# Performance work log

Measured on AMD Instinct MI355X. Metric: run time of the kernel, lower is better.

Reference implementation:

```python
import jax, jax.numpy as jnp
import numpy as np
from jax import lax

B, S, T = 64, 50, 50
U, E = 1024, 256
VI, VT = 12000, 16000
BOS = 1


def _gru_step(h, x, Wx, Wh, b):
    # Keras GRU v2 (reset_after=True): b[0]=input bias, b[1]=recurrent bias
    gi = x @ Wx + b[0]          # [B, 3U]
    gh = h @ Wh + b[1]          # [B, 3U]
    iz, ir, ih = jnp.split(gi, 3, axis=-1)
    hz, hr, hh = jnp.split(gh, 3, axis=-1)
    z = jax.nn.sigmoid(iz + hz)
    r = jax.nn.sigmoid(ir + hr)
    hcand = jnp.tanh(ih + r * hh)
    return z * h + (1.0 - z) * hcand


def setup_inputs() -> dict:
    key = jax.random.key(0)
    ks = jax.random.split(key, 20)
    f = lambda k, shp: (jax.random.normal(k, shp, dtype=jnp.float32) * 0.05)
    inp = jax.random.randint(ks[0], (B, S), 0, VI)
    targ = jax.random.randint(ks[1], (B, T), 0, VT)
    targ = targ.at[:, 0].set(BOS)  # <bos> first token (teacher forcing input)
    return {
        'inp': inp,
        'targ': targ,
        'enc_hidden': jnp.zeros((B, U), jnp.float32),
        'enc_emb': f(ks[2], (VI, E)),
        'enc_Wx': f(ks[3], (E, 3 * U)),
        'enc_Wh': f(ks[4], (U, 3 * U)),
        'enc_b': jnp.zeros((2, 3 * U), jnp.float32),
        'W1': f(ks[5], (U, U)), 'b1': jnp.zeros((U,), jnp.float32),
        'W2': f(ks[6], (U, U)), 'b2': jnp.zeros((U,), jnp.float32),
        'V': f(ks[7], (U, 1)), 'bV': jnp.zeros((1,), jnp.float32),
        'dec_emb': f(ks[8], (VT, E)),
        'dec_Wx': f(ks[9], (U + E, 3 * U)),
        'dec_Wh': f(ks[10], (U, 3 * U)),
        'dec_b': jnp.zeros((2, 3 * U), jnp.float32),
        'fc_W': f(ks[11], (U, VT)), 'fc_b': jnp.zeros((VT,), jnp.float32),
    }


def reference(inp, targ, enc_hidden, enc_emb, enc_Wx, enc_Wh, enc_b,
              W1, b1, W2, b2, V, bV,
              dec_emb, dec_Wx, dec_Wh, dec_b, fc_W, fc_b):
    # ----- encoder GRU over source -----
    xe = enc_emb[inp]                             # [B,S,E]
    def enc_step(h, xt):
        h2 = _gru_step(h, xt, enc_Wx, enc_Wh, enc_b)
        return h2, h2
    h_last, outs = lax.scan(enc_step, enc_hidden, xe.transpose(1, 0, 2))
    enc_out = outs.transpose(1, 0, 2)             # [B,S,U]

    # ----- teacher-forcing decode -----
    keys = enc_out @ W2 + b2                      # W2(values), precomputed [B,S,U]
    dec_in_emb = dec_emb[targ[:, :-1]]            # [B,T-1,E] (col 0 is <bos>)
    targets = targ[:, 1:]                         # [B,T-1]

    def dec_step(dh, inps):
        x_emb, yt = inps                          # [B,E], [B]
        # Bahdanau attention on dec_hidden
        s = jnp.tanh((dh @ W1 + b1)[:, None, :] + keys)   # [B,S,U]
        score = jnp.einsum('bsu,uo->bso', s, V) + bV      # [B,S,1]
        attn = jax.nn.softmax(score, axis=1)
        ctx = jnp.sum(attn * enc_out, axis=1)             # [B,U]
        x = jnp.concatenate([ctx, x_emb], axis=-1)        # [B,U+E]
        # original code calls gru(x) with NO initial state -> zero h_prev
        h_new = _gru_step(jnp.zeros_like(dh), x, dec_Wx, dec_Wh, dec_b)
        logits = h_new @ fc_W + fc_b                      # [B,VT]
        logp = jax.nn.log_softmax(logits, axis=-1)
        nll = -jnp.take_along_axis(logp, yt[:, None], axis=1)[:, 0]
        mask = (yt != 0).astype(nll.dtype)
        return h_new, jnp.mean(nll * mask)

    _, losses = lax.scan(dec_step, h_last,
                         (dec_in_emb.transpose(1, 0, 2), targets.T))
    return jnp.sum(losses)
```

## Files before the change

### kernel.cpp

```cpp
#include <hip/hip_runtime.h>
#include <cstdint>
#include <cstddef>

#define BB 64
#define SS 50
#define TT 50
#define TD 49
#define UU 1024
#define EE 256
#define VT 16000
#define G3 3072
#define MPAD 3200

using short8 = __attribute__((ext_vector_type(8))) short;
using short4v = __attribute__((ext_vector_type(4))) short;
using uint4v = __attribute__((ext_vector_type(4))) unsigned int;
using f32x4  = __attribute__((ext_vector_type(4))) float;

__device__ __forceinline__ short f2bf(float f) {
    uint32_t u = __float_as_uint(f);
    uint32_t r = (u + 0x7fffu + ((u >> 16) & 1u)) >> 16;
    return (short)r;
}
__device__ __forceinline__ float bf2f(short s) {
    return __uint_as_float(((uint32_t)(uint16_t)s) << 16);
}
__device__ __forceinline__ float sigm(float x) { return 1.0f / (1.0f + __expf(-x)); }
__device__ __forceinline__ float ftanh(float x) {
    float xc = fminf(fmaxf(x, -8.0f), 8.0f);
    float e = __expf(2.0f * xc);
    return (e - 1.0f) / (e + 1.0f);
}

__device__ __forceinline__ void vstore_bf(short* p, float v) { *(volatile short*)p = f2bf(v); }

__device__ __forceinline__ void gbar(int* flags, int* go, int t) {
    asm volatile("s_waitcnt vmcnt(0)" ::: "memory");
    __syncthreads();
    if (blockIdx.x == 0) {
        if (threadIdx.x < 64) {
            if (threadIdx.x == 0)
                __hip_atomic_store(&flags[0], t, __ATOMIC_RELAXED, __HIP_MEMORY_SCOPE_AGENT);
            int v;
            do {
                v = __hip_atomic_load(&flags[threadIdx.x], __ATOMIC_RELAXED, __HIP_MEMORY_SCOPE_AGENT);
            } while (__ballot(v >= t) != ~0ull);
            if (threadIdx.x == 0)
                __hip_atomic_store(go, t, __ATOMIC_RELAXED, __HIP_MEMORY_SCOPE_AGENT);
        }
    } else {
        if (threadIdx.x == 0) {
            __hip_atomic_store(&flags[blockIdx.x], t, __ATOMIC_RELAXED, __HIP_MEMORY_SCOPE_AGENT);
            while (__hip_atomic_load(go, __ATOMIC_RELAXED, __HIP_MEMORY_SCOPE_AGENT) < t)
                __builtin_amdgcn_s_sleep(1);
        }
    }
    __syncthreads();
    asm volatile("" ::: "memory");
}

typedef __attribute__((address_space(3))) void lds_vp;
typedef __attribute__((address_space(1))) void gl_vp;
__device__ __forceinline__ void gload16(void* lds, const void* g) {
    __builtin_amdgcn_global_load_lds((const gl_vp*)(uintptr_t)g,
                                     (lds_vp*)(uint32_t)(uintptr_t)lds,
                                     16, 0, 0);
}
__device__ __forceinline__ f32x4 mfma16(short8 a, short8 b, f32x4 c) {
    return __builtin_amdgcn_mfma_f32_16x16x32_bf16(a, b, c, 0, 0, 0);
}

template<int BM, int BN, int WM, int WN, bool OUT_BF16, int REMAP>
__global__ __launch_bounds__(256) void gemm_bf16(
    const short* __restrict__ A, const short* __restrict__ Bt,
    const float* __restrict__ bias, void* __restrict__ C, int N, int K,
    int lda, int ldb)
{
    constexpr int BK = 32;
    __shared__ __attribute__((aligned(16))) short As[BM * BK];
    __shared__ __attribute__((aligned(16))) short Bs[BN * BK];

    const int tid  = threadIdx.x;
    const int wave = tid >> 6;
    const int lane = tid & 63;
    const int l15  = lane & 15;
    const int quad = lane >> 4;
    const int wm = wave >> 1, wn = wave & 1;
    const int n0 = blockIdx.x * BN;
    const int m0 = blockIdx.y * BM;

    f32x4 acc[WM / 16][WN / 16];
    #pragma unroll
    for (int i = 0; i < WM / 16; ++i)
        #pragma unroll
        for (int j = 0; j < WN / 16; ++j)
            acc[i][j] = (f32x4)0.0f;

    for (int k0 = 0; k0 < K; k0 += BK) {
        #pragma unroll
        for (int it = 0; it < BM / 64; ++it) {
            int e = (it * 256 + tid) * 8;
            int row = e >> 5, col = e & 31;
            gload16(As + (it * 256 + wave * 64) * 8,
                    A + (size_t)(m0 + row) * lda + k0 + col);
        }
        #pragma unroll
        for (int it = 0; it < BN / 64; ++it) {
            int e = (it * 256 + tid) * 8;
            int row = e >> 5, col = e & 31;
            gload16(Bs + (it * 256 + wave * 64) * 8,
                    Bt + (size_t)(n0 + row) * ldb + k0 + col);
        }
        __syncthreads();
        short8 af[WM / 16], bfr[WN / 16];
        #pragma unroll
        for (int i = 0; i < WM / 16; ++i)
            af[i] = *(const short8*)(As + (wm * WM + i * 16 + l15) * BK + quad * 8);
        #pragma unroll
        for (int j = 0; j < WN / 16; ++j)
            bfr[j] = *(const short8*)(Bs + (wn * WN + j * 16 + l15) * BK + quad * 8);
        #pragma unroll
        for (int i = 0; i < WM / 16; ++i)
            #pragma unroll
            for (int j = 0; j < WN / 16; ++j)
                acc[i][j] = mfma16(af[i], bfr[j], acc[i][j]);
        __syncthreads();
    }

    #pragma unroll
    for (int i = 0; i < WM / 16; ++i) {
        #pragma unroll
        for (int j = 0; j < WN / 16; ++j) {
            int row = m0 + wm * WM + i * 16 + quad * 4;
            int col = n0 + wn * WN + j * 16 + l15;
            float bia = bias ? bias[col] : 0.0f;
            #pragma unroll
            for (int r = 0; r < 4; ++r) {
                size_t off;
                if (REMAP == 1)
                    off = ((size_t)((row + r) & 63) * SS + ((row + r) >> 6)) * N + col;
                else if (REMAP == 2)
                    off = (((size_t)((row + r) & 63) * SS + ((row + r) >> 6)) * UU
                           + (col & 1023)) * 4 + (col >> 10);
                else
                    off = (size_t)(row + r) * N + col;
                float v = acc[i][j][r] + bia;
                if (OUT_BF16) ((short*)C)[off] = f2bf(v);
                else          ((float*)C)[off] = v;
            }
        }
    }
}

__global__ __launch_bounds__(256) void transpose_bf(
    const float* __restrict__ in, short* __restrict__ out, int ldin, int ldout)
{
    __shared__ float tile[64][65];
    int n0 = blockIdx.x * 64, k0 = blockIdx.y * 64;
    int c = threadIdx.x & 63, rr = threadIdx.x >> 6;
    #pragma unroll 4
    for (int i = 0; i < 16; ++i) {
        int row = rr * 16 + i;
        tile[row][c] = in[(size_t)(k0 + row) * ldin + n0 + c];
    }
    __syncthreads();
    #pragma unroll 4
    for (int i = 0; i < 16; ++i) {
        int row = rr * 16 + i;
        out[(size_t)(n0 + row) * ldout + k0 + c] = f2bf(tile[c][row]);
    }
}

__global__ __launch_bounds__(256) void transpose_pack(
    const float* __restrict__ W, short* __restrict__ Wp, int N, int K)
{
    int lane = threadIdx.x & 63;
    int it = blockIdx.x * 4 + (threadIdx.x >> 6);
    int nt = blockIdx.y;
    int KI = K >> 5;
    int kb = it * 32 + (lane >> 4) * 8;
    int n  = nt * 16 + (lane & 15);
    short8 v;
    #pragma unroll
    for (int e = 0; e < 8; ++e)
        v[e] = f2bf(W[(size_t)(kb + e) * N + n]);
    *(short8*)(Wp + (((size_t)nt * KI + it) * 64 + lane) * 8) = v;
}

__global__ __launch_bounds__(256) void prep_gather(
    const int* __restrict__ inp, const int* __restrict__ targ,
    const float* __restrict__ enc_emb, const float* __restrict__ dec_emb,
    const float* __restrict__ enc_h0,
    short* __restrict__ Ae, short* __restrict__ Ad,
    short* __restrict__ H_bf, short* __restrict__ h0_bf,
    float* __restrict__ out, int* __restrict__ bar)
{
    int blk = blockIdx.x, tid = threadIdx.x;
    if (blk < MPAD) {
        int s = blk >> 6, b = blk & 63;
        int row = inp[b * SS + s];
        Ae[(size_t)blk * EE + tid] = f2bf(enc_emb[(size_t)row * EE + tid]);
    } else if (blk < 2 * MPAD) {
        int m = blk - MPAD;
        if (m < TD * BB) {
            int t = m >> 6, b = m & 63;
            int row = targ[b * TT + t];
            Ad[(size_t)m * EE + tid] = f2bf(dec_emb[(size_t)row * EE + tid]);
        } else {
            Ad[(size_t)m * EE + tid] = 0;
        }
    } else {
        int r = blk - 2 * MPAD;
        for (int u = tid; u < UU; u += 256) {
            H_bf[(size_t)(TD * BB + r) * UU + u] = 0;
            h0_bf[(size_t)r * UU + u] = f2bf(enc_h0[(size_t)r * UU + u]);
        }
        if (r == 0) {
            bar[tid] = 0;
            if (tid == 0) out[0] = 0.0f;
        }
    }
}

__global__ __launch_bounds__(1024) void enc_scan(
    const short* __restrict__ h0, const short* __restrict__ Whp,
    const short* __restrict__ gi, const float* __restrict__ bias2,
    short* __restrict__ eout, int* __restrict__ bar)
{
    const int j    = blockIdx.x;
    const int tid  = threadIdx.x;
    const int lane = tid & 63;
    const int l15  = lane & 15;
    const int quad = lane >> 4;
    const int wave = tid >> 6;
    const int bg   = wave & 3;
    const int kq   = wave >> 2;
    const int u    = j * 16 + l15;

    __shared__ f32x4 red[4][3][4][64];
    int* flags = bar;     int* go = bar + 64;

    const short* Bp0 = Whp + ((((size_t)(0 * 64 + j)) * 32 + kq * 8) * 64 + lane) * 8;
    const short* Bp1 = Whp + ((((size_t)(1 * 64 + j)) * 32 + kq * 8) * 64 + lane) * 8;
    const short* Bp2 = Whp + ((((size_t)(2 * 64 + j)) * 32 + kq * 8) * 64 + lane) * 8;
    const float bz = bias2[u], br = bias2[UU + u], bh = bias2[2 * UU + u];

    for (int t = 0; t < SS; ++t) {
        const short* A = t ? eout + (size_t)(t - 1) * BB * UU : h0;
        const short* Arow = A + (size_t)(bg * 16 + l15) * UU + kq * 256 + quad * 8;
        short8 af[8];
        #pragma unroll
        for (int i = 0; i < 8; ++i) af[i] = *(const short8*)(Arow + i * 32);
        f32x4 a0 = (f32x4)0.0f, a1 = (f32x4)0.0f, a2 = (f32x4)0.0f;
        #pragma unroll
        for (int i = 0; i < 8; ++i) {
            a0 = mfma16(af[i], *(const short8*)(Bp0 + i * 512), a0);
            a1 = mfma16(af[i], *(const short8*)(Bp1 + i * 512), a1);
            a2 = mfma16(af[i], *(const short8*)(Bp2 + i * 512), a2);
        }
        red[kq][0][bg][lane] = a0;
        red[kq][1][bg][lane] = a1;
        red[kq][2][bg][lane] = a2;
        __syncthreads();
        if (kq == 0) {
            f32x4 s0 = red[0][0][bg][lane] + red[1][0][bg][lane] + red[2][0][bg][lane] + red[3][0][bg][lane];
            f32x4 s1 = red[0][1][bg][lane] + red[1][1][bg][lane] + red[2][1][bg][lane] + red[3][1][bg][lane];
            f32x4 s2 = red[0][2][bg][lane] + red[1][2][bg][lane] + red[2][2][bg][lane] + red[3][2][bg][lane];
            const short* git = gi + (size_t)t * BB * G3;
            float hv[4];
            #pragma unroll
            for (int r = 0; r < 4; ++r) {
                int b = bg * 16 + quad * 4 + r;
                hv[r] = bf2f(A[(size_t)b * UU + u]);
            }
            #pragma unroll
            for (int r = 0; r < 4; ++r) {
                int b = bg * 16 + quad * 4 + r;
                const short* gb = git + (size_t)b * G3;
                float iz = bf2f(gb[u]), ir = bf2f(gb[UU + u]), ih = bf2f(gb[2 * UU + u]);
                float z  = sigm(iz + s0[r] + bz);
                float rr = sigm(ir + s1[r] + br);
                float hc = ftanh(ih + rr * (s2[r] + bh));
                vstore_bf(eout + (size_t)t * BB * UU + (size_t)b * UU + u,
                          z * hv[r] + (1.0f - z) * hc);
            }
        }
        if (t != SS - 1) gbar(flags, go, t + 1);
    }
}

__global__ __launch_bounds__(1024) void dec_scan(
    const short* __restrict__ eout, const short* __restrict__ W1p,
    const float* __restrict__ b1, const short* __restrict__ keyp,
    const float* __restrict__ Vw, const float* __restrict__ bV,
    const short* __restrict__ Pp4, const short* __restrict__ xg,
    const float* __restrict__ db1, short* __restrict__ q_t,
    short* __restrict__ Hbf, int* __restrict__ bar)
{
    const int j    = blockIdx.x;
    const int tid  = threadIdx.x;
    const int lane = tid & 63;
    const int l15  = lane & 15;
    const int quad = lane >> 4;
    const int wave = tid >> 6;
    const int bg   = wave & 3;
    const int kq   = wave >> 2;
    const int u    = j * 16 + l15;

    __shared__ f32x4 redq[4][4][64];
    __shared__ float sc[64];
    __shared__ float attnw[64];
    __shared__ __attribute__((aligned(16))) short Ws[32 * 512];
    __shared__ __attribute__((aligned(16))) short Ks[SS * UU];
    int* flags = bar + 128;  int* go = bar + 192;

    {
        const short* wsrc = W1p + (size_t)j * 32 * 512;
        for (int c = wave; c < 32; c += 16)
            gload16(Ws + (size_t)c * 512, wsrc + ((size_t)c * 64 + lane) * 8);
        const short* ksrc = keyp + (size_t)j * SS * UU;
        for (int c = wave; c < (SS * UU) / 512; c += 16)
            gload16(Ks + (size_t)c * 512, ksrc + ((size_t)c * 64 + lane) * 8);
        asm volatile("s_waitcnt vmcnt(0)" ::: "memory");
        __syncthreads();
    }

    const short* BpQ = Ws + (size_t)kq * 4096 + (size_t)lane * 8;
    const float b1v = b1[u];
    const float bV0 = bV[0];

    float Vl[16];
    #pragma unroll
    for (int e = 0; e < 16; e += 4)
        *(float4*)&Vl[e] = *(const float4*)(Vw + lane * 16 + e);

    const float dz3 = db1[tid], dr3 = db1[UU + tid], dh3 = db1[2 * UU + tid];
    const short* Pb = Pp4 + (size_t)j * SS * UU * 4;

    for (int t = 0; t < TD; ++t) {
        const short* dh = t ? Hbf + (size_t)(t - 1) * BB * UU
                            : eout + (size_t)(SS - 1) * BB * UU;
        short* qt = q_t + (size_t)t * BB * UU;
        {
            const short* Arow = dh + (size_t)(bg * 16 + l15) * UU + kq * 256 + quad * 8;
            short8 af[8];
            #pragma unroll
            for (int i = 0; i < 8; ++i) af[i] = *(const short8*)(Arow + i * 32);
            f32x4 aq = (f32x4)0.0f;
            #pragma unroll
            for (int i = 0; i < 8; ++i)
                aq = mfma16(af[i], *(const short8*)(BpQ + i * 512), aq);
            redq[kq][bg][lane] = aq;
        }
        __syncthreads();
        if (kq == 0) {
            f32x4 s = redq[0][bg][lane] + redq[1][bg][lane] + redq[2][bg][lane] + redq[3][bg][lane];
            #pragma unroll
            for (int r = 0; r < 4; ++r)
                vstore_bf(qt + (size_t)(bg * 16 + quad * 4 + r) * UU + u, s[r] + b1v);
        }
        gbar(flags, go, 2 * t + 1);
        {
            const int b = j;
            float ql[16];
            {
                short8 q0 = *(const short8*)(qt + (size_t)b * UU + lane * 16);
                short8 q1 = *(const short8*)(qt + (size_t)b * UU + lane * 16 + 8);
                #pragma unroll
                for (int e = 0; e < 8; ++e) { ql[e] = bf2f(q0[e]); ql[8 + e] = bf2f(q1[e]); }
            }
            for (int s = wave; s < SS; s += 16) {
                const short* kp = Ks + (size_t)s * UU + lane * 16;
                short8 k0 = *(const short8*)kp;
                short8 k1 = *(const short8*)(kp + 8);
                float p = 0.0f;
                #pragma unroll
                for (int e = 0; e < 8; ++e) p += Vl[e] * ftanh(ql[e] + bf2f(k0[e]));
                #pragma unroll
                for (int e = 0; e < 8; ++e) p += Vl[8 + e] * ftanh(ql[8 + e] + bf2f(k1[e]));
                #pragma unroll
                for (int off = 32; off; off >>= 1) p += __shfl_down(p, off);
                if (lane == 0) sc[s] = p + bV0;
            }
            __syncthreads();
            if (wave == 0) {
                float v = (lane < SS) ? sc[lane] : -1e30f;
                float m = v;
                #pragma unroll
                for (int off = 32; off; off >>= 1) m = fmaxf(m, __shfl_down(m, off));
                m = __shfl(m, 0);
                float e = (lane < SS) ? __expf(v - m) : 0.0f;
                float ss = e;
                #pragma unroll
                for (int off = 32; off; off >>= 1) ss += __shfl_down(ss, off);
                ss = __shfl(ss, 0);
                if (lane < SS) attnw[lane] = e / ss;
            }
            __syncthreads();
            const short* xb = xg + ((size_t)t * BB + b) * G3;
            float g0 = bf2f(xb[tid]);
            float g1 = bf2f(xb[UU + tid]);
            float g2 = bf2f(xb[2 * UU + tid]);
            const short* Pu = Pb + (size_t)tid * 4;
            #pragma unroll 10
            for (int s = 0; s < SS; ++s) {
                float w = attnw[s];
                short4v pv = *(const short4v*)(Pu + (size_t)s * UU * 4);
                g0 += w * bf2f(pv[0]);
                g1 += w * bf2f(pv[1]);
                g2 += w * bf2f(pv[2]);
            }
            float z  = sigm(g0 + dz3);
            float rr = sigm(g1 + dr3);
            float hc = ftanh(g2 + rr * dh3);
            vstore_bf(Hbf + ((size_t)t * BB + b) * UU + tid, (1.0f - z) * hc);
        }
        if (t != TD - 1) gbar(flags, go, 2 * t + 2);
    }
}

__global__ __launch_bounds__(256) void loss_kernel(
    const float* __restrict__ logits, const int* __restrict__ targ,
    int rows0, float* __restrict__ out)
{
    int gr = rows0 + blockIdx.x;
    int t = gr >> 6;
    if (t >= TD) return;
    int b = gr & 63;
    const float* lp = logits + (size_t)blockIdx.x * VT;
    int tid = threadIdx.x;
    __shared__ float redm[4], reds[4];

    float m = -INFINITY;
    for (int v = tid; v < VT; v += 256) m = fmaxf(m, lp[v]);
    #pragma unroll
    for (int off = 32; off; off >>= 1) m = fmaxf(m, __shfl_down(m, off));
    if ((tid & 63) == 0) redm[tid >> 6] = m;
    __syncthreads();
    float mm = fmaxf(fmaxf(redm[0], redm[1]), fmaxf(redm[2], redm[3]));

    float ssum = 0.0f;
    for (int v = tid; v < VT; v += 256) ssum += expf(lp[v] - mm);
    #pragma unroll
    for (int off = 32; off; off >>= 1) ssum += __shfl_down(ssum, off);
    if ((tid & 63) == 0) reds[tid >> 6] = ssum;
    __syncthreads();
    if (tid == 0) {
        float tot = reds[0] + reds[1] + reds[2] + reds[3];
        int y = targ[b * TT + t + 1];
        float nll = mm + logf(tot) - lp[y];
        if (y != 0) atomicAdd(out, nll * (1.0f / (float)BB));
    }
}

extern "C" void kernel_launch(void* const* d_in, const int* in_sizes, int n_in,
                              void* d_out, int out_size, void* d_ws, size_t ws_size,
                              hipStream_t stream)
{
    (void)in_sizes; (void)n_in; (void)out_size;
    const int*   inp      = (const int*)  d_in[0];
    const int*   targ     = (const int*)  d_in[1];
    const float* enc_h0   = (const float*)d_in[2];
    const float* enc_emb  = (const float*)d_in[3];
    const float* enc_Wx   = (const float*)d_in[4];
    const float* enc_Wh   = (const float*)d_in[5];
    const float* enc_b    = (const float*)d_in[6];
    const float* W1       = (const float*)d_in[7];
    const float* b1       = (const float*)d_in[8];
    const float* W2       = (const float*)d_in[9];
    const float* b2       = (const float*)d_in[10];
    const float* Vw       = (const float*)d_in[11];
    const float* bV       = (const float*)d_in[12];
    const float* dec_emb  = (const float*)d_in[13];
    const float* dec_Wx   = (const float*)d_in[14];
    const float* dec_b    = (const float*)d_in[16];
    const float* fc_W     = (const float*)d_in[17];
    const float* fc_b     = (const float*)d_in[18];
    float* out = (float*)d_out;

    char* p = (char*)d_ws;
    auto alloc = [&](size_t bytes) {
        char* r = (char*)(((uintptr_t)p + 255) & ~(uintptr_t)255);
        p = r + bytes;
        return r;
    };
    short* encWxt  = (short*)alloc((size_t)G3 * EE * 2);
    short* W2t     = (short*)alloc((size_t)UU * UU * 2);
    short* dWxt_c  = (short*)alloc((size_t)G3 * UU * 2);
    short* dWxt_e  = (short*)alloc((size_t)G3 * EE * 2);
    short* fcWt    = (short*)alloc((size_t)VT * UU * 2);
    short* encWhp  = (short*)alloc((size_t)G3 * UU * 2);
    short* W1p     = (short*)alloc((size_t)UU * UU * 2);
    short* Ae      = (short*)alloc((size_t)MPAD * EE * 2);
    short* Ad      = (short*)alloc((size_t)MPAD * EE * 2);
    short* enc_gi  = (short*)alloc((size_t)MPAD * G3 * 2);
    short* xemb_gi = (short*)alloc((size_t)MPAD * G3 * 2);
    short* enc_out = (short*)alloc((size_t)MPAD * UU * 2);
    short* keyp    = (short*)alloc((size_t)MPAD * UU * 2);
    short* Pp4     = (short*)alloc((size_t)MPAD * UU * 4 * 2);
    short* H_bf    = (short*)alloc((size_t)MPAD * UU * 2);
    short* h0_bf   = (short*)alloc((size_t)BB * UU * 2);
    short* q_t     = (short*)alloc((size_t)TD * BB * UU * 2);
    int*   bar     = (int*)alloc(256 * 4);

    size_t used = (size_t)(p - (char*)d_ws);
    size_t avail = (ws_size > used) ? ws_size - used : 0;
    int chunkRows = 640;
    while (chunkRows > 128 && (size_t)chunkRows * VT * 4 + 4096 > avail) chunkRows -= 128;
    float* logits = (float*)alloc((size_t)chunkRows * VT * 4);

    transpose_bf<<<dim3(G3/64, EE/64), 256, 0, stream>>>(enc_Wx, encWxt, G3, EE);
    transpose_bf<<<dim3(UU/64, UU/64), 256, 0, stream>>>(W2, W2t, UU, UU);
    transpose_bf<<<dim3(G3/64, UU/64), 256, 0, stream>>>(dec_Wx, dWxt_c, G3, UU);
    transpose_bf<<<dim3(G3/64, EE/64), 256, 0, stream>>>(dec_Wx + (size_t)UU * G3, dWxt_e, G3, EE);
    transpose_bf<<<dim3(VT/64, UU/64), 256, 0, stream>>>(fc_W, fcWt, VT, UU);
    transpose_pack<<<dim3(8, G3/16), 256, 0, stream>>>(enc_Wh, encWhp, G3, UU);
    transpose_pack<<<dim3(8, UU/16), 256, 0, stream>>>(W1, W1p, UU, UU);
    prep_gather<<<2 * MPAD + 64, 256, 0, stream>>>(inp, targ, enc_emb, dec_emb, enc_h0,
                                                   Ae, Ad, H_bf, h0_bf, out, bar);

    gemm_bf16<128,128,64,64,true,0><<<dim3(G3/128, MPAD/128), 256, 0, stream>>>(
        Ae, encWxt, enc_b, enc_gi, G3, EE, EE, EE);
    gemm_bf16<128,128,64,64,true,0><<<dim3(G3/128, MPAD/128), 256, 0, stream>>>(
        Ad, dWxt_e, dec_b, xemb_gi, G3, EE, EE, EE);

    {
        const short* a0 = h0_bf; const short* a1 = encWhp; const short* a2 = enc_gi;
        const float* a3 = enc_b + G3; short* a4 = enc_out; int* a5 = bar;
        void* args[] = {&a0, &a1, &a2, &a3, &a4, &a5};
        hipLaunchCooperativeKernel((void*)enc_scan, dim3(64), dim3(1024), args, 0, stream);
    }

    gemm_bf16<128,128,64,64,true,1><<<dim3(UU/128, MPAD/128), 256, 0, stream>>>(
        enc_out, W2t, b2, keyp, UU, UU, UU, UU);
    gemm_bf16<128,128,64,64,true,2><<<dim3(G3/128, MPAD/128), 256, 0, stream>>>(
        enc_out, dWxt_c, nullptr, Pp4, G3, UU, UU, UU);

    {
        const short* a0 = enc_out; const short* a1 = W1p; const float* a2 = b1;
        const short* a3 = keyp; const float* a4 = Vw; const float* a5 = bV;
        const short* a6 = Pp4; const short* a7 = xemb_gi; const float* a8 = dec_b + G3;
        short* a9 = q_t; short* a10 = H_bf; int* a11 = bar;
        void* args[] = {&a0, &a1, &a2, &a3, &a4, &a5, &a6, &a7, &a8, &a9, &a10, &a11};
        hipLaunchCooperativeKernel((void*)dec_scan, dim3(64), dim3(1024), args, 0, stream);
    }

    for (int rows0 = 0; rows0 < MPAD; rows0 += chunkRows) {
        int rows = MPAD - rows0; if (rows > chunkRows) rows = chunkRows;
        gemm_bf16<128,128,64,64,false,0><<<dim3(VT/128, rows/128), 256, 0, stream>>>(
            H_bf + (size_t)rows0 * UU, fcWt, fc_b, logits, VT, UU, UU, UU);
        loss_kernel<<<rows, 256, 0, stream>>>(logits, targ, rows0, out);
    }
}
```

Baseline: 2.586 ms.

## Fuse log-softmax partial stats into FC GEMM epilogue and spread GRU gate work

```diff
diff --git a/kernel.cpp b/kernel.cpp
--- a/kernel.cpp
+++ b/kernel.cpp
@@ -11,6 +11,7 @@
 #define VT 16000
 #define G3 3072
 #define MPAD 3200
+#define NCT 125
 
 using short8 = __attribute__((ext_vector_type(8))) short;
 using short4v = __attribute__((ext_vector_type(4))) short;
@@ -30,6 +31,9 @@
     float xc = fminf(fmaxf(x, -8.0f), 8.0f);
     float e = __expf(2.0f * xc);
     return (e - 1.0f) / (e + 1.0f);
+}
+__device__ __forceinline__ float vsel(f32x4 v, int k) {
+    return (k == 0) ? v[0] : (k == 1) ? v[1] : (k == 2) ? v[2] : v[3];
 }
 
 __device__ __forceinline__ void vstore_bf(short* p, float v) { *(volatile short*)p = f2bf(v); }
@@ -152,6 +156,135 @@
     }
 }
 
+__global__ __launch_bounds__(256) void fc_gemm(
+    const short* __restrict__ A, const short* __restrict__ Bt,
+    const float* __restrict__ bias, const int* __restrict__ targ,
+    float2* __restrict__ stats, float* __restrict__ tgtlog)
+{
+    constexpr int BM = 128, BN = 128, BK = 32;
+    __shared__ __attribute__((aligned(16))) short As[BM * BK];
+    __shared__ __attribute__((aligned(16))) short Bs[BN * BK];
+    __shared__ float2 st[BM][2];
+
+    const int tid  = threadIdx.x;
+    const int wave = tid >> 6;
+    const int lane = tid & 63;
+    const int l15  = lane & 15;
+    const int quad = lane >> 4;
+    const int wm = wave >> 1, wn = wave & 1;
+    const int n0 = blockIdx.x * BN;
+    const int m0 = blockIdx.y * BM;
+
+    f32x4 acc[4][4];
+    #pragma unroll
+    for (int i = 0; i < 4; ++i)
+        #pragma unroll
+        for (int j = 0; j < 4; ++j)
+            acc[i][j] = (f32x4)0.0f;
+
+    for (int k0 = 0; k0 < UU; k0 += BK) {
+        #pragma unroll
+        for (int it = 0; it < 2; ++it) {
+            int e = (it * 256 + tid) * 8;
+            int row = e >> 5, col = e & 31;
+            gload16(As + (it * 256 + wave * 64) * 8,
+                    A + (size_t)(m0 + row) * UU + k0 + col);
+            gload16(Bs + (it * 256 + wave * 64) * 8,
+                    Bt + (size_t)(n0 + row) * UU + k0 + col);
+        }
+        __syncthreads();
+        short8 af[4], bfr[4];
+        #pragma unroll
+        for (int i = 0; i < 4; ++i)
+            af[i] = *(const short8*)(As + (wm * 64 + i * 16 + l15) * BK + quad * 8);
+        #pragma unroll
+        for (int j = 0; j < 4; ++j)
+            bfr[j] = *(const short8*)(Bs + (wn * 64 + j * 16 + l15) * BK + quad * 8);
+        #pragma unroll
+        for (int i = 0; i < 4; ++i)
+            #pragma unroll
+            for (int j = 0; j < 4; ++j)
+                acc[i][j] = mfma16(af[i], bfr[j], acc[i][j]);
+        __syncthreads();
+    }
+
+    float bia[4];
+    #pragma unroll
+    for (int j = 0; j < 4; ++j)
+        bia[j] = bias[n0 + wn * 64 + j * 16 + l15];
+
+    #pragma unroll
+    for (int i = 0; i < 4; ++i) {
+        #pragma unroll
+        for (int r = 0; r < 4; ++r) {
+            float v0 = acc[i][0][r] + bia[0];
+            float v1 = acc[i][1][r] + bia[1];
+            float v2 = acc[i][2][r] + bia[2];
+            float v3 = acc[i][3][r] + bia[3];
+            float mx = fmaxf(fmaxf(v0, v1), fmaxf(v2, v3));
+            #pragma unroll
+            for (int off = 1; off < 16; off <<= 1)
+                mx = fmaxf(mx, __shfl_xor(mx, off));
+            float se = __expf(v0 - mx) + __expf(v1 - mx)
+                     + __expf(v2 - mx) + __expf(v3 - mx);
+            #pragma unroll
+            for (int off = 1; off < 16; off <<= 1)
+                se += __shfl_xor(se, off);
+            int rowt = wm * 64 + i * 16 + quad * 4 + r;
+            if (l15 == 0) st[rowt][wn] = make_float2(mx, se);
+            int grow = m0 + rowt;
+            int tt = grow >> 6, bb = grow & 63;
+            if (tt < TD) {
+                int y = targ[bb * TT + tt + 1];
+                int yl = y - n0;
+                if (yl >= 0 && yl < BN && (yl >> 6) == wn && (yl & 15) == l15) {
+                    int jy = (yl >> 4) & 3;
+                    float tv = (jy == 0) ? v0 : (jy == 1) ? v1 : (jy == 2) ? v2 : v3;
+                    tgtlog[grow] = tv;
+                }
+            }
+        }
+    }
+    __syncthreads();
+    if (tid < BM) {
+        float2 a2 = st[tid][0], b2 = st[tid][1];
+        float M = fmaxf(a2.x, b2.x);
+        float S = a2.y * __expf(a2.x - M) + b2.y * __expf(b2.x - M);
+        stats[(size_t)(m0 + tid) * NCT + blockIdx.x] = make_float2(M, S);
+    }
+}
+
+__global__ __launch_bounds__(64) void loss_combine(
+    const float2* __restrict__ stats, const float* __restrict__ tgtlog,
+    const int* __restrict__ targ, float* __restrict__ out)
+{
+    int grow = blockIdx.x;
+    int tid = threadIdx.x;
+    const float2* sp = stats + (size_t)grow * NCT;
+    float2 e0 = sp[tid];
+    float M = e0.x, S = e0.y;
+    if (tid + 64 < NCT) {
+        float2 e1 = sp[tid + 64];
+        float Mn = fmaxf(M, e1.x);
+        S = S * __expf(M - Mn) + e1.y * __expf(e1.x - Mn);
+        M = Mn;
+    }
+    #pragma unroll
+    for (int off = 32; off; off >>= 1) {
+        float Mo = __shfl_down(M, off);
+        float So = __shfl_down(S, off);
+        float Mn = fmaxf(M, Mo);
+        S = S * __expf(M - Mn) + So * __expf(Mo - Mn);
+        M = Mn;
+    }
+    if (tid == 0) {
+        int tt = grow >> 6, bb = grow & 63;
+        int y = targ[bb * TT + tt + 1];
+        float nll = M + logf(S) - tgtlog[grow];
+        if (y != 0) atomicAdd(out, nll * (1.0f / (float)BB));
+    }
+}
+
 __global__ __launch_bounds__(256) void transpose_bf(
     const float* __restrict__ in, short* __restrict__ out, int ldin, int ldout)
 {
@@ -262,28 +395,21 @@
         red[kq][1][bg][lane] = a1;
         red[kq][2][bg][lane] = a2;
         __syncthreads();
-        if (kq == 0) {
+        {
             f32x4 s0 = red[0][0][bg][lane] + red[1][0][bg][lane] + red[2][0][bg][lane] + red[3][0][bg][lane];
             f32x4 s1 = red[0][1][bg][lane] + red[1][1][bg][lane] + red[2][1][bg][lane] + red[3][1][bg][lane];
             f32x4 s2 = red[0][2][bg][lane] + red[1][2][bg][lane] + red[2][2][bg][lane] + red[3][2][bg][lane];
-            const short* git = gi + (size_t)t * BB * G3;
-            float hv[4];
-            #pragma unroll
-            for (int r = 0; r < 4; ++r) {
-                int b = bg * 16 + quad * 4 + r;
-                hv[r] = bf2f(A[(size_t)b * UU + u]);
-            }
-            #pragma unroll
-            for (int r = 0; r < 4; ++r) {
-                int b = bg * 16 + quad * 4 + r;
-                const short* gb = git + (size_t)b * G3;
-                float iz = bf2f(gb[u]), ir = bf2f(gb[UU + u]), ih = bf2f(gb[2 * UU + u]);
-                float z  = sigm(iz + s0[r] + bz);
-                float rr = sigm(ir + s1[r] + br);
-                float hc = ftanh(ih + rr * (s2[r] + bh));
-                vstore_bf(eout + (size_t)t * BB * UU + (size_t)b * UU + u,
-                          z * hv[r] + (1.0f - z) * hc);
-            }
+            const int r = kq;
+            const int b = bg * 16 + quad * 4 + r;
+            float s0v = vsel(s0, r), s1v = vsel(s1, r), s2v = vsel(s2, r);
+            float hv = bf2f(A[(size_t)b * UU + u]);
+            const short* gb = gi + (size_t)t * BB * G3 + (size_t)b * G3;
+            float iz = bf2f(gb[u]), ir = bf2f(gb[UU + u]), ih = bf2f(gb[2 * UU + u]);
+            float z  = sigm(iz + s0v + bz);
+            float rr = sigm(ir + s1v + br);
+            float hc = ftanh(ih + rr * (s2v + bh));
+            vstore_bf(eout + (size_t)t * BB * UU + (size_t)b * UU + u,
+                      z * hv + (1.0f - z) * hc);
         }
         if (t != SS - 1) gbar(flags, go, t + 1);
     }
@@ -353,11 +479,10 @@
             redq[kq][bg][lane] = aq;
         }
         __syncthreads();
-        if (kq == 0) {
+        {
             f32x4 s = redq[0][bg][lane] + redq[1][bg][lane] + redq[2][bg][lane] + redq[3][bg][lane];
-            #pragma unroll
-            for (int r = 0; r < 4; ++r)
-                vstore_bf(qt + (size_t)(bg * 16 + quad * 4 + r) * UU + u, s[r] + b1v);
+            float sv = vsel(s, kq);
+            vstore_bf(qt + (size_t)(bg * 16 + quad * 4 + kq) * UU + u, sv + b1v);
         }
         gbar(flags, go, 2 * t + 1);
         {
@@ -419,45 +544,11 @@
     }
 }
 
-__global__ __launch_bounds__(256) void loss_kernel(
-    const float* __restrict__ logits, const int* __restrict__ targ,
-    int rows0, float* __restrict__ out)
-{
-    int gr = rows0 + blockIdx.x;
-    int t = gr >> 6;
-    if (t >= TD) return;
-    int b = gr & 63;
-    const float* lp = logits + (size_t)blockIdx.x * VT;
-    int tid = threadIdx.x;
-    __shared__ float redm[4], reds[4];
-
-    float m = -INFINITY;
-    for (int v = tid; v < VT; v += 256) m = fmaxf(m, lp[v]);
-    #pragma unroll
-    for (int off = 32; off; off >>= 1) m = fmaxf(m, __shfl_down(m, off));
-    if ((tid & 63) == 0) redm[tid >> 6] = m;
-    __syncthreads();
-    float mm = fmaxf(fmaxf(redm[0], redm[1]), fmaxf(redm[2], redm[3]));
-
-    float ssum = 0.0f;
-    for (int v = tid; v < VT; v += 256) ssum += expf(lp[v] - mm);
-    #pragma unroll
-    for (int off = 32; off; off >>= 1) ssum += __shfl_down(ssum, off);
-    if ((tid & 63) == 0) reds[tid >> 6] = ssum;
-    __syncthreads();
-    if (tid == 0) {
-        float tot = reds[0] + reds[1] + reds[2] + reds[3];
-        int y = targ[b * TT + t + 1];
-        float nll = mm + logf(tot) - lp[y];
-        if (y != 0) atomicAdd(out, nll * (1.0f / (float)BB));
-    }
-}
-
 extern "C" void kernel_launch(void* const* d_in, const int* in_sizes, int n_in,
                               void* d_out, int out_size, void* d_ws, size_t ws_size,
                               hipStream_t stream)
 {
-    (void)in_sizes; (void)n_in; (void)out_size;
+    (void)in_sizes; (void)n_in; (void)out_size; (void)ws_size;
     const int*   inp      = (const int*)  d_in[0];
     const int*   targ     = (const int*)  d_in[1];
     const float* enc_h0   = (const float*)d_in[2];
@@ -502,12 +593,8 @@
     short* h0_bf   = (short*)alloc((size_t)BB * UU * 2);
     short* q_t     = (short*)alloc((size_t)TD * BB * UU * 2);
     int*   bar     = (int*)alloc(256 * 4);
-
-    size_t used = (size_t)(p - (char*)d_ws);
-    size_t avail = (ws_size > used) ? ws_size - used : 0;
-    int chunkRows = 640;
-    while (chunkRows > 128 && (size_t)chunkRows * VT * 4 + 4096 > avail) chunkRows -= 128;
-    float* logits = (float*)alloc((size_t)chunkRows * VT * 4);
+    float2* stats  = (float2*)alloc((size_t)MPAD * NCT * sizeof(float2));
+    float* tgtlog  = (float*)alloc((size_t)MPAD * 4);
 
     transpose_bf<<<dim3(G3/64, EE/64), 256, 0, stream>>>(enc_Wx, encWxt, G3, EE);
     transpose_bf<<<dim3(UU/64, UU/64), 256, 0, stream>>>(W2, W2t, UU, UU);
@@ -545,10 +632,7 @@
         hipLaunchCooperativeKernel((void*)dec_scan, dim3(64), dim3(1024), args, 0, stream);
     }
 
-    for (int rows0 = 0; rows0 < MPAD; rows0 += chunkRows) {
-        int rows = MPAD - rows0; if (rows > chunkRows) rows = chunkRows;
-        gemm_bf16<128,128,64,64,false,0><<<dim3(VT/128, rows/128), 256, 0, stream>>>(
-            H_bf + (size_t)rows0 * UU, fcWt, fc_b, logits, VT, UU, UU, UU);
-        loss_kernel<<<rows, 256, 0, stream>>>(logits, targ, rows0, out);
-    }
-}
+    fc_gemm<<<dim3(VT/128, MPAD/128), 256, 0, stream>>>(
+        H_bf, fcWt, fc_b, targ, stats, tgtlog);
+    loss_combine<<<TD * BB, 64, 0, stream>>>(stats, tgtlog, targ, out);
+}
```

Measured after the change: 2.343 ms. 1.1x faster.
